# Performance work log

Measured on AMD Instinct MI355X. Metric: run time of the kernel, lower is better.

The kernel has to match this reference:

```python
import jax, jax.numpy as jnp
import numpy as np

B, L = 4096, 200
N_USERS, N_ITEMS, N_CATS, N_DUR = 200000, 500000, 1000, 20
D = 64  # item_embed_dim == seq_embed_dim


def _lin(k, din, dout):
    kw, kb = jax.random.split(k)
    s = 1.0 / np.sqrt(din)
    return (jax.random.uniform(kw, (din, dout), minval=-s, maxval=s),
            jax.random.uniform(kb, (dout,), minval=-s, maxval=s))


def setup_inputs() -> dict:
    key = jax.random.key(0)
    ks = jax.random.split(key, 20)
    inp = {
        'user_id': jax.random.randint(ks[0], (B,), 0, N_USERS),
        'item_id': jax.random.randint(ks[1], (B,), 0, N_ITEMS),
        'item_category': jax.random.randint(ks[2], (B,), 0, N_CATS),
        'item_dur_bkt': jax.random.randint(ks[3], (B,), 0, N_DUR),
        'user_dense': jax.random.normal(ks[4], (B, 25), dtype=jnp.float32),
        'item_dense': jax.random.normal(ks[5], (B, 3), dtype=jnp.float32),
        'history_seq': jax.random.randint(ks[6], (B, L), 0, N_ITEMS + 1),
        # embedding tables (init std=0.01 as in _init_weights)
        'user_W': 0.01 * jax.random.normal(ks[7], (N_USERS, 64), dtype=jnp.float32),
        'item_W': 0.01 * jax.random.normal(ks[8], (N_ITEMS, D), dtype=jnp.float32),
        'cat_W': 0.01 * jax.random.normal(ks[9], (N_CATS, 16), dtype=jnp.float32),
        'dur_W': 0.01 * jax.random.normal(ks[10], (N_DUR, 8), dtype=jnp.float32),
        'hist_W': 0.01 * jax.random.normal(ks[11], (N_ITEMS + 1, D), dtype=jnp.float32),
    }
    # attention MLP: 4*D=256 -> 64 -> 32 -> 1
    inp['aW0'], inp['ab0'] = _lin(ks[12], 4 * D, 64)
    inp['aW1'], inp['ab1'] = _lin(ks[13], 64, 32)
    inp['aW2'], inp['ab2'] = _lin(ks[14], 32, 1)
    # final MLP: concat_dim 64+64+16+8+25+3+64 = 244 -> 256 -> 128 -> 1
    inp['mW0'], inp['mb0'] = _lin(ks[15], 244, 256)
    inp['mW1'], inp['mb1'] = _lin(ks[16], 256, 128)
    inp['mW2'], inp['mb2'] = _lin(ks[17], 128, 1)
    return inp


def reference(user_id, item_id, item_category, item_dur_bkt, user_dense, item_dense,
              history_seq, user_W, item_W, cat_W, dur_W, hist_W,
              aW0, ab0, aW1, ab1, aW2, ab2, mW0, mb0, mW1, mb1, mW2, mb2):
    u_emb = user_W[user_id]            # (B, 64)
    i_emb = item_W[item_id]            # (B, D)
    c_emb = cat_W[item_category]       # (B, 16)
    d_emb = dur_W[item_dur_bkt]        # (B, 8)
    hist = hist_W[history_seq]         # (B, L, D)

    t = i_emb[:, None, :]              # (B, 1, D); item_dim == seq_dim so no slice
    tb = jnp.broadcast_to(t, hist.shape)
    feat = jnp.concatenate([hist, tb, hist * t, hist - t], axis=-1)  # (B, L, 4D)

    h = jax.nn.relu(feat @ aW0 + ab0)
    h = jax.nn.relu(h @ aW1 + ab1)
    scores = (h @ aW2 + ab2)[..., 0]   # (B, L)

    pad_mask = history_seq == 0
    scores = jnp.where(pad_mask, jnp.float32(-1e9), scores)
    w = jax.nn.softmax(scores, axis=-1)                # (B, L)
    pooled = jnp.einsum('bl,bld->bd', w, hist)         # (B, D)

    x = jnp.concatenate([u_emb, i_emb, c_emb, d_emb, user_dense, item_dense, pooled], axis=-1)
    h = jax.nn.relu(x @ mW0 + mb0)     # dropout is identity in eval mode
    h = jax.nn.relu(h @ mW1 + mb1)
    logit = (h @ mW2 + mb2)[..., 0]
    return jax.nn.sigmoid(logit)       # (B,)
```

## Files before the change

kernel.cpp:

```cpp
#include <hip/hip_runtime.h>

#define L_SZ 200
#define RB 8
#define HS_STRIDE 72

typedef __attribute__((ext_vector_type(8))) short short8;
typedef __attribute__((ext_vector_type(4))) float floatx4;

__device__ __forceinline__ unsigned short f2bf(float f) {
    unsigned int u = __float_as_uint(f);
    unsigned int r = (u + 0x7fffu + ((u >> 16) & 1u)) >> 16;
    return (unsigned short)r;
}
__device__ __forceinline__ float bf2f(unsigned short h) {
    return __uint_as_float(((unsigned int)h) << 16);
}
__device__ __forceinline__ float wave_sum64(float v) {
    #pragma unroll
    for (int m = 1; m <= 32; m <<= 1) v += __shfl_xor(v, m, 64);
    return v;
}
__device__ __forceinline__ float wave_max64(float v) {
    #pragma unroll
    for (int m = 1; m <= 32; m <<= 1) v = fmaxf(v, __shfl_xor(v, m, 64));
    return v;
}
__device__ __forceinline__ unsigned int pk2(float a, float b) {
    return ((unsigned int)f2bf(b) << 16) | (unsigned int)f2bf(a);
}

__global__ __launch_bounds__(256) void prep_kernel(
    const int* __restrict__ item_id, const float* __restrict__ item_W,
    const float* __restrict__ aW0, const float* __restrict__ ab0,
    const float* __restrict__ aW1,
    float* __restrict__ T1t, float* __restrict__ T2t,
    unsigned short* __restrict__ PW1, float* __restrict__ cb_ws)
{
    __shared__ float shbuf[3 * 64 * 65];
    const int tid = threadIdx.x;
    if (blockIdx.x == 0) {
        #pragma unroll
        for (int t = 0; t < 3; ++t) {
            const int r0 = (t == 0) ? 0 : (t == 1) ? 128 : 192;
            for (int u = tid; u < 1024; u += 256) {
                int k = u >> 4, c4 = u & 15;
                float4 v = *(const float4*)(aW0 + (r0 + k) * 64 + c4 * 4);
                float* dst = shbuf + t * 4160 + k * 65 + c4 * 4;
                dst[0] = v.x; dst[1] = v.y; dst[2] = v.z; dst[3] = v.w;
            }
        }
        __syncthreads();
        for (int u = tid; u < 4096; u += 256) {
            int j = u >> 6, k = u & 63;
            T1t[u] = shbuf[k * 65 + j] + shbuf[2 * 4160 + k * 65 + j];
            T2t[u] = shbuf[4160 + k * 65 + j];
        }
        for (int u = tid; u < 2048; u += 256) {
            int i = u & 7, lane = (u >> 3) & 63, f = u >> 9;
            int nt = f >> 1, ks = f & 1;
            int k = ks * 32 + (lane >> 4) * 8 + i;
            int n = nt * 16 + (lane & 15);
            PW1[u] = f2bf(aW1[k * 32 + n]);
        }
    } else {
        for (int u = tid; u < 4096; u += 256) {
            int k = u >> 6, j = u & 63;
            shbuf[k * 65 + j] = aW0[(64 + k) * 64 + j] - aW0[(192 + k) * 64 + j];
        }
        __syncthreads();
        const int bl = tid >> 6, j = tid & 63;
        const int b = (blockIdx.x - 1) * 4 + bl;
        const float* ie = item_W + (size_t)item_id[b] * 64;
        float acc = ab0[j];
        #pragma unroll 8
        for (int k = 0; k < 64; ++k) acc = fmaf(ie[k], shbuf[k * 65 + j], acc);
        cb_ws[(size_t)b * 64 + j] = acc;
    }
}

__global__ __launch_bounds__(256, 4) void attn_kernel(
    const int* __restrict__ item_id, const int* __restrict__ hist_seq,
    const float* __restrict__ item_W, const float* __restrict__ hist_W,
    const float* __restrict__ T1t, const float* __restrict__ T2t,
    const unsigned short* __restrict__ PW1, const float* __restrict__ cb_ws,
    const float* __restrict__ ab1, const float* __restrict__ aW2,
    const float* __restrict__ ab2, float* __restrict__ pooled_ws)
{
    __shared__ __align__(16) unsigned char smem[38624];
    unsigned short* Hs  = (unsigned short*)(smem);
    unsigned short* BB  = (unsigned short*)(smem + 28800);
    int*   seq_sh = (int*)(smem + 36992);
    float* scores = (float*)(smem + 37792);
    float* red    = (float*)(smem + 38592);

    const int tid  = threadIdx.x;
    const int w    = tid >> 6;
    const int lane = tid & 63;
    const int b    = blockIdx.x;
    const int* hseq = hist_seq + b * L_SZ;

    if (tid < L_SZ) seq_sh[tid] = hseq[tid];

    const int rbase = tid >> 3, c8 = tid & 7;
    const bool extra = tid < 64;
    const int r6 = extra ? 192 + rbase : 0;
    const float* sp[7];
    #pragma unroll
    for (int t = 0; t < 6; ++t)
        sp[t] = hist_W + (size_t)hseq[rbase + t * 32] * 64 + c8 * 8;
    sp[6] = hist_W + (size_t)hseq[r6] * 64 + c8 * 8;
    float4 f0[7], f1[7];
    #pragma unroll
    for (int t = 0; t < 7; ++t) {
        f0[t] = *(const float4*)sp[t];
        f1[t] = *(const float4*)(sp[t] + 4);
    }

    const int c = lane & 15, q = lane >> 4;
    short8 bW1[2][2];
    #pragma unroll
    for (int nt = 0; nt < 2; ++nt)
        #pragma unroll
        for (int ks = 0; ks < 2; ++ks)
            bW1[nt][ks] = *(const short8*)(PW1 + ((nt * 2 + ks) * 64 + lane) * 8);
    float cbr[4];
    #pragma unroll
    for (int nt = 0; nt < 4; ++nt) cbr[nt] = cb_ws[(size_t)b * 64 + nt * 16 + c];
    float ab1r[2], aw2r[2];
    #pragma unroll
    for (int nt = 0; nt < 2; ++nt) {
        ab1r[nt] = ab1[nt * 16 + c];
        aw2r[nt] = aW2[nt * 16 + c];
    }
    const float ab2s = ab2[0];

    #pragma unroll
    for (int t = 0; t < 6; ++t) {
        uint4 pk;
        pk.x = pk2(f0[t].x, f0[t].y); pk.y = pk2(f0[t].z, f0[t].w);
        pk.z = pk2(f1[t].x, f1[t].y); pk.w = pk2(f1[t].z, f1[t].w);
        *(uint4*)(Hs + (rbase + t * 32) * HS_STRIDE + c8 * 8) = pk;
    }
    if (extra) {
        uint4 pk;
        pk.x = pk2(f0[6].x, f0[6].y); pk.y = pk2(f0[6].z, f0[6].w);
        pk.z = pk2(f1[6].x, f1[6].y); pk.w = pk2(f1[6].z, f1[6].w);
        *(uint4*)(Hs + r6 * HS_STRIDE + c8 * 8) = pk;
    }

    {
        const float* irow = item_W + (size_t)item_id[b] * 64;
        const int j0 = tid >> 3;
        float4 em0 = *(const float4*)(irow + c8 * 8);
        float4 em1 = *(const float4*)(irow + c8 * 8 + 4);
        #pragma unroll
        for (int t = 0; t < 2; ++t) {
            int j = j0 + t * 32;
            const float* p1 = T1t + j * 64 + c8 * 8;
            const float* p2 = T2t + j * 64 + c8 * 8;
            float4 a0 = *(const float4*)p1, a1 = *(const float4*)(p1 + 4);
            float4 b0 = *(const float4*)p2, b1 = *(const float4*)(p2 + 4);
            float v[8];
            v[0] = a0.x + em0.x * b0.x; v[1] = a0.y + em0.y * b0.y;
            v[2] = a0.z + em0.z * b0.z; v[3] = a0.w + em0.w * b0.w;
            v[4] = a1.x + em1.x * b1.x; v[5] = a1.y + em1.y * b1.y;
            v[6] = a1.z + em1.z * b1.z; v[7] = a1.w + em1.w * b1.w;
            uint4 pk;
            pk.x = pk2(v[0], v[1]); pk.y = pk2(v[2], v[3]);
            pk.z = pk2(v[4], v[5]); pk.w = pk2(v[6], v[7]);
            *(uint4*)(BB + j * 64 + (c8 ^ (j & 7)) * 8) = pk;
        }
    }
    __syncthreads();

    short8 bW[4][2];
    #pragma unroll
    for (int nt = 0; nt < 4; ++nt)
        #pragma unroll
        for (int ks = 0; ks < 2; ++ks)
            bW[nt][ks] = *(const short8*)(BB + (nt * 16 + c) * 64
                                             + ((4 * ks + q) ^ (c & 7)) * 8);
    __syncthreads();

    unsigned short* scrw = BB + w * (16 * 64);
    const floatx4 zf = {0.f, 0.f, 0.f, 0.f};

    for (int mt = w; mt < 13; mt += 4) {
        const int rowbase = mt * 16;
        floatx4 acc0[4] = {zf, zf, zf, zf};
        #pragma unroll
        for (int ks = 0; ks < 2; ++ks) {
            short8 a = *(const short8*)(Hs + (rowbase + c) * HS_STRIDE + ks * 32 + q * 8);
            acc0[0] = __builtin_amdgcn_mfma_f32_16x16x32_bf16(a, bW[0][ks], acc0[0], 0, 0, 0);
            acc0[1] = __builtin_amdgcn_mfma_f32_16x16x32_bf16(a, bW[1][ks], acc0[1], 0, 0, 0);
            acc0[2] = __builtin_amdgcn_mfma_f32_16x16x32_bf16(a, bW[2][ks], acc0[2], 0, 0, 0);
            acc0[3] = __builtin_amdgcn_mfma_f32_16x16x32_bf16(a, bW[3][ks], acc0[3], 0, 0, 0);
        }
        #pragma unroll
        for (int nt = 0; nt < 4; ++nt)
            #pragma unroll
            for (int r = 0; r < 4; ++r) {
                float h = fmaxf(acc0[nt][r] + cbr[nt], 0.f);
                int row = q * 4 + r;
                int gp = (2 * nt + (c >> 3)) ^ (row & 7);
                scrw[row * 64 + gp * 8 + (c & 7)] = f2bf(h);
            }
        floatx4 acc1[2] = {zf, zf};
        #pragma unroll
        for (int ks = 0; ks < 2; ++ks) {
            short8 a1 = *(const short8*)(scrw + c * 64 + ((4 * ks + q) ^ (c & 7)) * 8);
            acc1[0] = __builtin_amdgcn_mfma_f32_16x16x32_bf16(a1, bW1[0][ks], acc1[0], 0, 0, 0);
            acc1[1] = __builtin_amdgcn_mfma_f32_16x16x32_bf16(a1, bW1[1][ks], acc1[1], 0, 0, 0);
        }
        float s[4];
        #pragma unroll
        for (int r = 0; r < 4; ++r)
            s[r] = fmaxf(acc1[0][r] + ab1r[0], 0.f) * aw2r[0]
                 + fmaxf(acc1[1][r] + ab1r[1], 0.f) * aw2r[1];
        #pragma unroll
        for (int m = 1; m <= 8; m <<= 1)
            #pragma unroll
            for (int r = 0; r < 4; ++r) s[r] += __shfl_xor(s[r], m, 64);
        if (c == 0) {
            #pragma unroll
            for (int r = 0; r < 4; ++r) {
                int l = rowbase + q * 4 + r;
                if (l < L_SZ)
                    scores[l] = (seq_sh[l] == 0) ? -1.0e9f : (s[r] + ab2s);
            }
        }
    }
    __syncthreads();

    float s0 = (tid < L_SZ) ? scores[tid] : -3.0e38f;
    float mx = wave_max64(s0);
    if (lane == 0) red[w] = mx;
    __syncthreads();
    mx = fmaxf(fmaxf(red[0], red[1]), fmaxf(red[2], red[3]));
    float e = (tid < L_SZ) ? __expf(s0 - mx) : 0.f;
    float sm = wave_sum64(e);
    if (lane == 0) red[4 + w] = sm;
    __syncthreads();
    const float winv = 1.f / ((red[4] + red[5]) + (red[6] + red[7]));
    if (tid < L_SZ) scores[tid] = e * winv;
    __syncthreads();

    float* pools = (float*)BB;
    {
        int g  = (w << 1) | (lane >> 5);
        int jj = lane & 31;
        int l0 = g * 26, l1 = (l0 + 26 < L_SZ) ? l0 + 26 : L_SZ;
        float p0 = 0.f, p1 = 0.f;
        for (int l = l0; l < l1; ++l) {
            float wt = scores[l];
            unsigned int pv = *(const unsigned int*)(Hs + l * HS_STRIDE + jj * 2);
            p0 = fmaf(wt, bf2f((unsigned short)(pv & 0xffffu)), p0);
            p1 = fmaf(wt, bf2f((unsigned short)(pv >> 16)), p1);
        }
        float2 pp = {p0, p1};
        *(float2*)&pools[g * 64 + jj * 2] = pp;
    }
    __syncthreads();
    if (tid < 64) {
        float sum = 0.f;
        #pragma unroll
        for (int g = 0; g < 8; ++g) sum += pools[g * 64 + tid];
        pooled_ws[(size_t)b * 64 + tid] = sum;
    }
}

__global__ __launch_bounds__(256) void mlp_kernel(
    const int* __restrict__ user_id, const int* __restrict__ item_id,
    const int* __restrict__ item_cat, const int* __restrict__ item_dur,
    const float* __restrict__ user_dense, const float* __restrict__ item_dense,
    const float* __restrict__ user_W, const float* __restrict__ item_W,
    const float* __restrict__ cat_W, const float* __restrict__ dur_W,
    const float* __restrict__ mW0, const float* __restrict__ mb0,
    const float* __restrict__ mW1, const float* __restrict__ mb1,
    const float* __restrict__ mW2, const float* __restrict__ mb2,
    const float* __restrict__ pooled_ws, float* __restrict__ out)
{
    __shared__ __align__(16) float xT[244][RB];
    __shared__ __align__(16) float h0T[256][RB];
    __shared__ __align__(16) float h1T[128][RB];
    __shared__ __align__(16) float part[128][RB];

    const int tid = threadIdx.x;
    const int b0 = blockIdx.x * RB;

    for (int idx = tid; idx < 244 * RB; idx += 256) {
        int r = idx / 244;
        int c = idx - r * 244;
        int b = b0 + r;
        float v;
        if (c < 64)       v = user_W[(size_t)user_id[b] * 64 + c];
        else if (c < 128) v = item_W[(size_t)item_id[b] * 64 + (c - 64)];
        else if (c < 144) v = cat_W[item_cat[b] * 16 + (c - 128)];
        else if (c < 152) v = dur_W[item_dur[b] * 8 + (c - 144)];
        else if (c < 177) v = user_dense[b * 25 + (c - 152)];
        else if (c < 180) v = item_dense[b * 3 + (c - 177)];
        else              v = pooled_ws[(size_t)b * 64 + (c - 180)];
        xT[c][r] = v;
    }
    __syncthreads();

    {
        float acc[RB];
        const float bias = mb0[tid];
        #pragma unroll
        for (int r = 0; r < RB; ++r) acc[r] = bias;
        #pragma unroll 4
        for (int k = 0; k < 244; ++k) {
            float wk = mW0[k * 256 + tid];
            float4 xa = *(const float4*)&xT[k][0];
            float4 xb = *(const float4*)&xT[k][4];
            acc[0] = fmaf(wk, xa.x, acc[0]);
            acc[1] = fmaf(wk, xa.y, acc[1]);
            acc[2] = fmaf(wk, xa.z, acc[2]);
            acc[3] = fmaf(wk, xa.w, acc[3]);
            acc[4] = fmaf(wk, xb.x, acc[4]);
            acc[5] = fmaf(wk, xb.y, acc[5]);
            acc[6] = fmaf(wk, xb.z, acc[6]);
            acc[7] = fmaf(wk, xb.w, acc[7]);
        }
        #pragma unroll
        for (int r = 0; r < RB; ++r) h0T[tid][r] = fmaxf(acc[r], 0.f);
    }
    __syncthreads();

    const int jj = tid & 127;
    const int half = tid >> 7;
    {
        float acc[RB];
        #pragma unroll
        for (int r = 0; r < RB; ++r) acc[r] = 0.f;
        #pragma unroll 4
        for (int t = 0; t < 128; ++t) {
            int k = half * 128 + t;
            float wk = mW1[k * 128 + jj];
            float4 ha = *(const float4*)&h0T[k][0];
            float4 hb = *(const float4*)&h0T[k][4];
            acc[0] = fmaf(wk, ha.x, acc[0]);
            acc[1] = fmaf(wk, ha.y, acc[1]);
            acc[2] = fmaf(wk, ha.z, acc[2]);
            acc[3] = fmaf(wk, ha.w, acc[3]);
            acc[4] = fmaf(wk, hb.x, acc[4]);
            acc[5] = fmaf(wk, hb.y, acc[5]);
            acc[6] = fmaf(wk, hb.z, acc[6]);
            acc[7] = fmaf(wk, hb.w, acc[7]);
        }
        if (half == 1) {
            #pragma unroll
            for (int r = 0; r < RB; ++r) part[jj][r] = acc[r];
        }
        __syncthreads();
        if (half == 0) {
            const float bias = mb1[jj];
            #pragma unroll
            for (int r = 0; r < RB; ++r)
                h1T[jj][r] = fmaxf(acc[r] + part[jj][r] + bias, 0.f);
        }
    }
    __syncthreads();

    if (tid < RB) {
        const int r = tid;
        float a0 = mb2[0], a1 = 0.f;
        #pragma unroll 8
        for (int k = 0; k < 128; k += 2) {
            a0 = fmaf(h1T[k][r],     mW2[k],     a0);
            a1 = fmaf(h1T[k + 1][r], mW2[k + 1], a1);
        }
        float a = a0 + a1;
        out[b0 + r] = 1.f / (1.f + __expf(-a));
    }
}

extern "C" void kernel_launch(void* const* d_in, const int* in_sizes, int n_in,
                              void* d_out, int out_size, void* d_ws, size_t ws_size,
                              hipStream_t stream) {
    (void)in_sizes; (void)n_in; (void)out_size; (void)ws_size;
    const int*   user_id    = (const int*)d_in[0];
    const int*   item_id    = (const int*)d_in[1];
    const int*   item_cat   = (const int*)d_in[2];
    const int*   item_dur   = (const int*)d_in[3];
    const float* user_dense = (const float*)d_in[4];
    const float* item_dense = (const float*)d_in[5];
    const int*   hist_seq   = (const int*)d_in[6];
    const float* user_W     = (const float*)d_in[7];
    const float* item_W     = (const float*)d_in[8];
    const float* cat_W      = (const float*)d_in[9];
    const float* dur_W      = (const float*)d_in[10];
    const float* hist_W     = (const float*)d_in[11];
    const float* aW0 = (const float*)d_in[12];
    const float* ab0 = (const float*)d_in[13];
    const float* aW1 = (const float*)d_in[14];
    const float* ab1 = (const float*)d_in[15];
    const float* aW2 = (const float*)d_in[16];
    const float* ab2 = (const float*)d_in[17];
    const float* mW0 = (const float*)d_in[18];
    const float* mb0 = (const float*)d_in[19];
    const float* mW1 = (const float*)d_in[20];
    const float* mb1 = (const float*)d_in[21];
    const float* mW2 = (const float*)d_in[22];
    const float* mb2 = (const float*)d_in[23];
    float* out = (float*)d_out;

    char* ws = (char*)d_ws;
    float* pooled_ws = (float*)ws;
    float* cb_ws     = (float*)(ws + (1u << 20));
    float* T1t       = (float*)(ws + (2u << 20));
    float* T2t       = (float*)(ws + (2u << 20) + 16384);
    unsigned short* PW1 = (unsigned short*)(ws + (2u << 20) + 32768);

    prep_kernel<<<1025, 256, 0, stream>>>(item_id, item_W, aW0, ab0, aW1,
                                          T1t, T2t, PW1, cb_ws);
    attn_kernel<<<4096, 256, 0, stream>>>(item_id, hist_seq, item_W, hist_W,
                                          T1t, T2t, PW1, cb_ws,
                                          ab1, aW2, ab2, pooled_ws);
    mlp_kernel<<<4096 / RB, 256, 0, stream>>>(user_id, item_id, item_cat, item_dur,
                                              user_dense, item_dense,
                                              user_W, item_W, cat_W, dur_W,
                                              mW0, mb0, mW1, mb1, mW2, mb2,
                                              pooled_ws, out);
}
```

Measured before the change: 388.7 us.

## Use hardware bf16 pack, LDS-only barriers, and batch prep over 64 items per block

Replaces the software bf16 rounding pack with the v_cvt_pk_bf16_f32 instruction and uses it when writing the layer-0 activations in pairs. Swaps __syncthreads in the attention kernel for an lgkmcnt-only wait plus s_barrier, so barriers do not wait on outstanding global memory operations. Restructures the prep kernel so each of 64 blocks stages 64 item embeddings in LDS and reuses the aW0 difference matrix across them, instead of launching 1024 blocks that each rebuild that matrix. The custom barrier relies on no global stores being needed across barriers, and the prep kernel now runs on far fewer blocks.

```diff
diff --git a/kernel.cpp b/kernel.cpp
--- a/kernel.cpp
+++ b/kernel.cpp
@@ -15,6 +15,11 @@
 __device__ __forceinline__ float bf2f(unsigned short h) {
     return __uint_as_float(((unsigned int)h) << 16);
 }
+__device__ __forceinline__ unsigned int pk2(float a, float b) {
+    unsigned int r;
+    asm("v_cvt_pk_bf16_f32 %0, %1, %2" : "=v"(r) : "v"(a), "v"(b));
+    return r;
+}
 __device__ __forceinline__ float wave_sum64(float v) {
     #pragma unroll
     for (int m = 1; m <= 32; m <<= 1) v += __shfl_xor(v, m, 64);
@@ -25,8 +30,10 @@
     for (int m = 1; m <= 32; m <<= 1) v = fmaxf(v, __shfl_xor(v, m, 64));
     return v;
 }
-__device__ __forceinline__ unsigned int pk2(float a, float b) {
-    return ((unsigned int)f2bf(b) << 16) | (unsigned int)f2bf(a);
+__device__ __forceinline__ void bar_lds() {
+    asm volatile("s_waitcnt lgkmcnt(0)" ::: "memory");
+    __builtin_amdgcn_s_barrier();
+    asm volatile("" ::: "memory");
 }
 
 __global__ __launch_bounds__(256) void prep_kernel(
@@ -63,18 +70,27 @@
             PW1[u] = f2bf(aW1[k * 32 + n]);
         }
     } else {
+        float* T3 = shbuf;
+        float* IE = shbuf + 64 * 65;
+        const int B0 = (blockIdx.x - 1) * 64;
         for (int u = tid; u < 4096; u += 256) {
             int k = u >> 6, j = u & 63;
-            shbuf[k * 65 + j] = aW0[(64 + k) * 64 + j] - aW0[(192 + k) * 64 + j];
+            T3[k * 65 + j] = aW0[(64 + k) * 64 + j] - aW0[(192 + k) * 64 + j];
+        }
+        for (int u = tid; u < 4096; u += 256) {
+            int r = u >> 6, j = u & 63;
+            IE[r * 64 + j] = item_W[(size_t)item_id[B0 + r] * 64 + j];
         }
         __syncthreads();
-        const int bl = tid >> 6, j = tid & 63;
-        const int b = (blockIdx.x - 1) * 4 + bl;
-        const float* ie = item_W + (size_t)item_id[b] * 64;
-        float acc = ab0[j];
-        #pragma unroll 8
-        for (int k = 0; k < 64; ++k) acc = fmaf(ie[k], shbuf[k * 65 + j], acc);
-        cb_ws[(size_t)b * 64 + j] = acc;
+        const int j = tid & 63, rg = tid >> 6;
+        for (int pass = 0; pass < 16; ++pass) {
+            int bl = rg * 16 + pass;
+            float acc = ab0[j];
+            #pragma unroll 8
+            for (int k = 0; k < 64; ++k)
+                acc = fmaf(IE[bl * 64 + k], T3[k * 65 + j], acc);
+            cb_ws[(size_t)(B0 + bl) * 64 + j] = acc;
+        }
     }
 }
 
@@ -171,7 +187,7 @@
             *(uint4*)(BB + j * 64 + (c8 ^ (j & 7)) * 8) = pk;
         }
     }
-    __syncthreads();
+    bar_lds();
 
     short8 bW[4][2];
     #pragma unroll
@@ -180,7 +196,7 @@
         for (int ks = 0; ks < 2; ++ks)
             bW[nt][ks] = *(const short8*)(BB + (nt * 16 + c) * 64
                                              + ((4 * ks + q) ^ (c & 7)) * 8);
-    __syncthreads();
+    bar_lds();
 
     unsigned short* scrw = BB + w * (16 * 64);
     const floatx4 zf = {0.f, 0.f, 0.f, 0.f};
@@ -199,11 +215,16 @@
         #pragma unroll
         for (int nt = 0; nt < 4; ++nt)
             #pragma unroll
-            for (int r = 0; r < 4; ++r) {
-                float h = fmaxf(acc0[nt][r] + cbr[nt], 0.f);
-                int row = q * 4 + r;
-                int gp = (2 * nt + (c >> 3)) ^ (row & 7);
-                scrw[row * 64 + gp * 8 + (c & 7)] = f2bf(h);
+            for (int r = 0; r < 4; r += 2) {
+                float h0 = fmaxf(acc0[nt][r]     + cbr[nt], 0.f);
+                float h1 = fmaxf(acc0[nt][r + 1] + cbr[nt], 0.f);
+                unsigned int u = pk2(h0, h1);
+                int row0 = q * 4 + r;
+                int row1 = row0 + 1;
+                int gp0 = (2 * nt + (c >> 3)) ^ (row0 & 7);
+                int gp1 = (2 * nt + (c >> 3)) ^ (row1 & 7);
+                scrw[row0 * 64 + gp0 * 8 + (c & 7)] = (unsigned short)u;
+                scrw[row1 * 64 + gp1 * 8 + (c & 7)] = (unsigned short)(u >> 16);
             }
         floatx4 acc1[2] = {zf, zf};
         #pragma unroll
@@ -230,20 +251,20 @@
             }
         }
     }
-    __syncthreads();
+    bar_lds();
 
     float s0 = (tid < L_SZ) ? scores[tid] : -3.0e38f;
     float mx = wave_max64(s0);
     if (lane == 0) red[w] = mx;
-    __syncthreads();
+    bar_lds();
     mx = fmaxf(fmaxf(red[0], red[1]), fmaxf(red[2], red[3]));
     float e = (tid < L_SZ) ? __expf(s0 - mx) : 0.f;
     float sm = wave_sum64(e);
     if (lane == 0) red[4 + w] = sm;
-    __syncthreads();
+    bar_lds();
     const float winv = 1.f / ((red[4] + red[5]) + (red[6] + red[7]));
     if (tid < L_SZ) scores[tid] = e * winv;
-    __syncthreads();
+    bar_lds();
 
     float* pools = (float*)BB;
     {
@@ -260,7 +281,7 @@
         float2 pp = {p0, p1};
         *(float2*)&pools[g * 64 + jj * 2] = pp;
     }
-    __syncthreads();
+    bar_lds();
     if (tid < 64) {
         float sum = 0.f;
         #pragma unroll
@@ -413,8 +434,8 @@
     float* T2t       = (float*)(ws + (2u << 20) + 16384);
     unsigned short* PW1 = (unsigned short*)(ws + (2u << 20) + 32768);
 
-    prep_kernel<<<1025, 256, 0, stream>>>(item_id, item_W, aW0, ab0, aW1,
-                                          T1t, T2t, PW1, cb_ws);
+    prep_kernel<<<65, 256, 0, stream>>>(item_id, item_W, aW0, ab0, aW1,
+                                        T1t, T2t, PW1, cb_ws);
     attn_kernel<<<4096, 256, 0, stream>>>(item_id, hist_seq, item_W, hist_W,
                                           T1t, T2t, PW1, cb_ws,
                                           ab1, aW2, ab2, pooled_ws);
```

Measured after the change: 398.7 us. 1.03x slower.
